# Kernel tuning notes

Hardware: AMD Instinct MI355X
Metric: run time of the kernel (lower is better)

Reference implementation:

```python
import jax, jax.numpy as jnp
import numpy as np

B, T, E, H, L = 2, 2048, 1024, 16, 4
HD = E // H
FF = 4 * E


def setup_inputs() -> dict:
    key = jax.random.key(0)
    ks = jax.random.split(key, 9)
    s = 0.02
    return {
        "x": jax.random.normal(ks[0], (B, T, E), dtype=jnp.float32),
        "Wqkv": jax.random.normal(ks[1], (L, E, 3 * E), dtype=jnp.float32) * s,
        "bqkv": jnp.zeros((L, 3 * E), dtype=jnp.float32),
        "Wproj": jax.random.normal(ks[2], (L, E, E), dtype=jnp.float32) * s,
        "bproj": jnp.zeros((L, E), dtype=jnp.float32),
        "W1": jax.random.normal(ks[3], (L, E, FF), dtype=jnp.float32) * s,
        "b1": jnp.zeros((L, FF), dtype=jnp.float32),
        "W2": jax.random.normal(ks[4], (L, FF, E), dtype=jnp.float32) * s,
        "b2": jnp.zeros((L, E), dtype=jnp.float32),
    }


def _attention(x, Wqkv_l, bqkv_l, Wproj_l, bproj_l):
    # (B,T,E) -> (B,T,E); manual softmax attention as in source
    qkv = x @ Wqkv_l + bqkv_l                      # (B,T,3E)
    q, k, v = jnp.split(qkv, 3, axis=-1)
    q = q.reshape(B, T, H, HD).transpose(0, 2, 1, 3)  # (B,H,T,HD)
    k = k.reshape(B, T, H, HD).transpose(0, 2, 1, 3)
    v = v.reshape(B, T, H, HD).transpose(0, 2, 1, 3)
    att = jnp.einsum("bhqd,bhkd->bhqk", q, k) * (1.0 / np.sqrt(HD))
    att = jax.nn.softmax(att, axis=-1)             # (B,H,T,T)
    y = jnp.einsum("bhqk,bhkd->bhqd", att, v)      # (B,H,T,HD)
    y = y.transpose(0, 2, 1, 3).reshape(B, T, E)
    return y @ Wproj_l + bproj_l


def reference(x, Wqkv, bqkv, Wproj, bproj, W1, b1, W2, b2):
    for l in range(L):
        x = x + _attention(x, Wqkv[l], bqkv[l], Wproj[l], bproj[l])  # residual x+f(x)
        h = jax.nn.gelu(x @ W1[l] + b1[l]) @ W2[l] + b2[l]           # MLP block
        x = x + h
    return x
```

## Files before the change

kernel.cpp:

```cpp
#include <hip/hip_runtime.h>
#include <hip/hip_bf16.h>

#define B_  2
#define T_  2048
#define E_  1024
#define H_  16
#define HD_ 64
#define FF_ 4096
#define L_  4
#define M_  (B_*T_)
#define RS_ (3*E_)

typedef unsigned short u16;
typedef __attribute__((ext_vector_type(8))) short  short8;
typedef __attribute__((ext_vector_type(4))) float  f32x4;

#define QS 0.18033688011112042f

__device__ __forceinline__ u16 f2bf(float f) {
    union { float f; unsigned u; } v; v.f = f;
    unsigned r = (v.u + 0x7fffu + ((v.u >> 16) & 1u)) >> 16;
    return (u16)r;
}
__device__ __forceinline__ u16 f2bf_trunc(float f) {
    union { float f; unsigned u; } v; v.f = f;
    return (u16)(v.u >> 16);
}

__device__ __forceinline__ void gll16(const u16* g, u16* lds) {
    __builtin_amdgcn_global_load_lds(
        (const __attribute__((address_space(1))) unsigned int*)g,
        (__attribute__((address_space(3))) unsigned int*)lds, 16, 0, 0);
}

__global__ __launch_bounds__(256) void transpose_weights(
    const float* __restrict__ Wqkv, const float* __restrict__ Wproj,
    const float* __restrict__ W1,   const float* __restrict__ W2,
    u16* __restrict__ WT) {
    __shared__ float tile[32][33];
    int bid = blockIdx.x;
    const float* src; u16* dst; int K, N, lt;
    if (bid < 3072)      { src = Wqkv;  dst = WT;           K = 1024; N = 3072; lt = bid;        }
    else if (bid < 4096) { src = Wproj; dst = WT + 3145728; K = 1024; N = 1024; lt = bid - 3072; }
    else if (bid < 8192) { src = W1;    dst = WT + 4194304; K = 1024; N = 4096; lt = bid - 4096; }
    else                 { src = W2;    dst = WT + 8388608; K = 4096; N = 1024; lt = bid - 8192; }
    int tpr = N >> 5;
    int ti = lt / tpr, tj = lt % tpr;
    int k0 = ti << 5, n0 = tj << 5;
    int tx = threadIdx.x & 31, ty = threadIdx.x >> 5;
    for (int i = 0; i < 4; i++) {
        int r = ty + (i << 3);
        tile[r][tx] = src[(size_t)(k0 + r) * N + n0 + tx];
    }
    __syncthreads();
    for (int i = 0; i < 4; i++) {
        int r = ty + (i << 3);
        dst[(size_t)(n0 + r) * K + k0 + tx] = f2bf(tile[tx][r]);
    }
}

__global__ __launch_bounds__(256) void convert_kernel(
    const float* __restrict__ in, u16* __restrict__ out, int n4) {
    int i = blockIdx.x * 256 + threadIdx.x;
    if (i < n4) {
        float4 v = ((const float4*)in)[i];
        ushort4 w;
        w.x = f2bf(v.x); w.y = f2bf(v.y); w.z = f2bf(v.z); w.w = f2bf(v.w);
        ((ushort4*)out)[i] = w;
    }
}

template <int EPI>
__global__ __launch_bounds__(512, 4) void gemm_fat(
    const u16* __restrict__ A, const u16* __restrict__ Bt,
    const float* __restrict__ bias, u16* __restrict__ outp,
    int N, int K) {
    __shared__ u16 As[3][128 * 32];
    __shared__ u16 Bs[3][256 * 32];
    int t = threadIdx.x;
    int wid = t >> 6, lane = t & 63;
    int l15 = t & 15, quad = (t >> 4) & 3;
    int wr = wid >> 2, wc = wid & 3;

    int nbx = N >> 8;
    int nwg = nbx << 5;
    int flat = blockIdx.x;
    int q = nwg >> 3;
    int gid = (flat & 7) * q + (flat >> 3);
    int within = gid & 127;
    int m0 = (within >> 2) << 7;
    int n0 = (((gid >> 7) << 2) + (within & 3)) << 8;

    f32x4 acc[4][4];
#pragma unroll
    for (int i = 0; i < 4; i++)
#pragma unroll
        for (int j = 0; j < 4; j++) acc[i][j] = (f32x4){0.f, 0.f, 0.f, 0.f};

    int srow = t >> 2;
    int kch  = (((lane & 3) ^ ((lane >> 3) & 3)) << 3);
    const u16* gA  = &A [(size_t)(m0 + srow) * K + kch];
    const u16* gB0 = &Bt[(size_t)(n0 + srow) * K + kch];
    const u16* gB1 = gB0 + (size_t)128 * K;

    int xo = (l15 >> 1) & 3;
    int abase = (((wr << 6) + l15) << 5) + ((quad ^ xo) << 3);
    int bbase = (((wc << 6) + l15) << 5) + ((quad ^ xo) << 3);

    int nk = K >> 5;

#define STAGE_FAT(buf, ko) do {                                              \
        gll16(gA  + (ko), &As[buf][(wid << 4) << 5]);                        \
        gll16(gB0 + (ko), &Bs[buf][(wid << 4) << 5]);                        \
        gll16(gB1 + (ko), &Bs[buf][((wid << 4) + 128) << 5]);                \
    } while (0)

    STAGE_FAT(0, 0);
    STAGE_FAT(1, 32);

    for (int kk = 0; kk < nk; kk++) {
        if (kk < nk - 1) asm volatile("s_waitcnt vmcnt(3)" ::: "memory");
        else             asm volatile("s_waitcnt vmcnt(0)" ::: "memory");
        __builtin_amdgcn_s_barrier();
        __builtin_amdgcn_sched_barrier(0);

        if (kk + 2 < nk) STAGE_FAT((kk + 2) % 3, (kk + 2) << 5);

        const u16* as = &As[kk % 3][0];
        const u16* bs = &Bs[kk % 3][0];
        short8 af[4], bfr[4];
#pragma unroll
        for (int i = 0; i < 4; i++)
            af[i] = *(const short8*)(as + abase + (i << 9));
#pragma unroll
        for (int j = 0; j < 4; j++)
            bfr[j] = *(const short8*)(bs + bbase + (j << 9));
#pragma unroll
        for (int i = 0; i < 4; i++)
#pragma unroll
            for (int j = 0; j < 4; j++)
                acc[i][j] = __builtin_amdgcn_mfma_f32_16x16x32_bf16(af[i], bfr[j], acc[i][j], 0, 0, 0);
    }
#undef STAGE_FAT

#pragma unroll
    for (int j = 0; j < 4; j++) {
        int gn = n0 + (wc << 6) + (j << 4) + l15;
        float bv = bias[gn];
#pragma unroll
        for (int i = 0; i < 4; i++) {
            int mb = m0 + (wr << 6) + (i << 4) + (quad << 2);
#pragma unroll
            for (int r = 0; r < 4; r++) {
                size_t idx = (size_t)(mb + r) * N + gn;
                float v = acc[i][j][r] + bv;
                if (EPI == 0) {
                    if (gn < E_) v *= QS;
                    outp[idx] = f2bf(v);
                } else {
                    float u  = 0.7978845608028654f * (v + 0.044715f * v * v * v);
                    float th = 1.f - 2.f / (__expf(2.f * u) + 1.f);
                    outp[idx] = f2bf(0.5f * v * (1.f + th));
                }
            }
        }
    }
}

__global__ __launch_bounds__(256) void gemm_n64(
    const u16* __restrict__ A, const u16* __restrict__ Bt,
    const float* __restrict__ bias, const float* __restrict__ res,
    float* __restrict__ outp, u16* __restrict__ out2, int M, int N, int K) {
    __shared__ u16 As[3][128 * 32];
    __shared__ u16 Bs[3][64 * 32];
    int t = threadIdx.x;
    int wid = t >> 6, lane = t & 63;
    int flat = blockIdx.y * gridDim.x + blockIdx.x;
    int gid = ((flat & 7) << 6) + (flat >> 3);
    int within = gid & 127;
    int m0 = (within >> 2) << 7;
    int n0 = (((gid >> 7) << 2) + (within & 3)) << 6;
    int l15 = t & 15, quad = (t >> 4) & 3;
    int wr = wid >> 1, wc = wid & 1;
    f32x4 acc[4][2];
#pragma unroll
    for (int i = 0; i < 4; i++)
#pragma unroll
        for (int j = 0; j < 2; j++) acc[i][j] = (f32x4){0.f, 0.f, 0.f, 0.f};

    int kch = (((lane & 3) ^ ((lane >> 3) & 3)) << 3);
    const u16* gA = &A [(size_t)(m0 + (wid << 5) + (lane >> 2)) * K + kch];
    const u16* gB = &Bt[(size_t)(n0 + (wid << 4) + (lane >> 2)) * K + kch];

    int xo = (l15 >> 1) & 3;
    int abase = (((wr << 6) + l15) << 5) + ((quad ^ xo) << 3);
    int bbase = (((wc << 5) + l15) << 5) + ((quad ^ xo) << 3);

    int nk = K >> 5;

#define STAGE_N64(buf, ko) do {                                              \
        gll16(gA + (ko),                    &As[buf][(wid << 5) << 5]);      \
        gll16(gA + (ko) + (size_t)16 * K,   &As[buf][((wid << 5) + 16) << 5]); \
        gll16(gB + (ko),                    &Bs[buf][(wid << 4) << 5]);      \
    } while (0)

    STAGE_N64(0, 0);
    STAGE_N64(1, 32);

    for (int kk = 0; kk < nk; kk++) {
        if (kk < nk - 1) asm volatile("s_waitcnt vmcnt(3)" ::: "memory");
        else             asm volatile("s_waitcnt vmcnt(0)" ::: "memory");
        __builtin_amdgcn_s_barrier();
        __builtin_amdgcn_sched_barrier(0);

        if (kk + 2 < nk) STAGE_N64((kk + 2) % 3, (kk + 2) << 5);

        const u16* as = &As[kk % 3][0];
        const u16* bs = &Bs[kk % 3][0];
        short8 af[4], bfr[2];
#pragma unroll
        for (int i = 0; i < 4; i++)
            af[i] = *(const short8*)(as + abase + (i << 9));
#pragma unroll
        for (int j = 0; j < 2; j++)
            bfr[j] = *(const short8*)(bs + bbase + (j << 9));
#pragma unroll
        for (int i = 0; i < 4; i++)
#pragma unroll
            for (int j = 0; j < 2; j++)
                acc[i][j] = __builtin_amdgcn_mfma_f32_16x16x32_bf16(
                    af[i], bfr[j], acc[i][j], 0, 0, 0);
    }
#undef STAGE_N64

#pragma unroll
    for (int j = 0; j < 2; j++) {
        int gn = n0 + (wc << 5) + (j << 4) + l15;
        float bv = bias[gn];
#pragma unroll
        for (int i = 0; i < 4; i++) {
            int mb = m0 + (wr << 6) + (i << 4) + (quad << 2);
#pragma unroll
            for (int r = 0; r < 4; r++) {
                size_t idx = (size_t)(mb + r) * N + gn;
                float o = acc[i][j][r] + bv + res[idx];
                outp[idx] = o;
                out2[idx] = f2bf(o);
            }
        }
    }
}

__global__ __launch_bounds__(256) void attn_kernel(
    const u16* __restrict__ qkv, u16* __restrict__ y) {
    __shared__ u16 Ks[2][64 * 64];
    __shared__ u16 Vt[2][64 * 64];
    __shared__ u16 Pb[4][16 * 64];

    int t = threadIdx.x;
    int q0 = blockIdx.x << 6;
    int h  = blockIdx.y;
    int b  = blockIdx.z;
    const u16* bq = qkv + (size_t)b * T_ * RS_;

    int wid = t >> 6, lane = t & 63, l15 = t & 15, quad = (t >> 4) & 3;
    int sw = l15 & 7;
    int ro0 = (l15 << 6) + ((quad ^ sw) << 3);
    int ro1 = ro0 ^ 32;
    int krow = (wid << 4) + (lane >> 3);
    size_t kg0 = (size_t)krow * RS_ + E_ + h * 64 + (((lane & 7) ^ (lane >> 3)) << 3);
    int vkp = t & 31, vdc = t >> 5;
    size_t vg0 = (size_t)(2 * vkp) * RS_ + 2 * E_ + h * 64 + (vdc << 3);
    int vwo[8];
#pragma unroll
    for (int i = 0; i < 8; i++)
        vwo[i] = (((vdc << 3) + i) << 6) + ((((vkp >> 2) ^ i)) << 3) + ((vkp & 3) << 1);
    int pwo[4];
#pragma unroll
    for (int kt = 0; kt < 4; kt++)
        pwo[kt] = (l15 << 6) + ((((kt << 1) | (quad >> 1)) ^ sw) << 3) + ((quad & 1) << 2);
    u16* pw = &Pb[wid][0];

    const u16* qp = bq + (size_t)(q0 + (wid << 4) + l15) * RS_ + h * 64;
    short8 qf0 = *(const short8*)(qp + (quad << 3));
    short8 qf1 = *(const short8*)(qp + (quad << 3) + 32);

    float l = 0.f;
    f32x4 o[4];
#pragma unroll
    for (int dt = 0; dt < 4; dt++) o[dt] = (f32x4){0.f, 0.f, 0.f, 0.f};

    gll16(bq + kg0,            &Ks[0][(wid << 4) << 6]);
    gll16(bq + kg0 + 8 * RS_,  &Ks[0][((wid << 4) + 8) << 6]);
    {
        union { uint4 q; u16 u[8]; } a_, b_;
        a_.q = *(const uint4*)(bq + vg0);
        b_.q = *(const uint4*)(bq + vg0 + RS_);
#pragma unroll
        for (int i = 0; i < 8; i++) {
            unsigned pk = (unsigned)a_.u[i] | ((unsigned)b_.u[i] << 16);
            *(unsigned*)(&Vt[0][0] + vwo[i]) = pk;
        }
    }

#define ATTN_CHUNK(KSB, VTB, KSN, VTN, C0) do {                                \
    __syncthreads();                           \
    int cn_ = (C0) + 64;                                                       \
    uint4 v0_, v1_;                                                            \
    bool pf_ = (cn_ < T_);                                                     \
    if (pf_) {                                                                 \
        size_t cb_ = (size_t)cn_ * RS_;                                        \
        gll16(bq + cb_ + kg0,           (KSN) + ((wid << 4) << 6));            \
        gll16(bq + cb_ + kg0 + 8 * RS_, (KSN) + (((wid << 4) + 8) << 6));      \
        v0_ = *(const uint4*)(bq + cb_ + vg0);                                 \
        v1_ = *(const uint4*)(bq + cb_ + vg0 + RS_);                           \
    }                                                                          \
    f32x4 s_[4];                                                               \
    _Pragma("unroll")                                                          \
    for (int kt = 0; kt < 4; kt++) {                                           \
        short8 ka0 = *(const short8*)((KSB) + (kt << 10) + ro0);               \
        short8 ka1 = *(const short8*)((KSB) + (kt << 10) + ro1);               \
        f32x4 z = (f32x4){0.f, 0.f, 0.f, 0.f};                                 \
        z = __builtin_amdgcn_mfma_f32_16x16x32_bf16(ka0, qf0, z, 0, 0, 0);     \
        z = __builtin_amdgcn_mfma_f32_16x16x32_bf16(ka1, qf1, z, 0, 0, 0);     \
        s_[kt] = z;                                                            \
    }                                                                          \
    float rsum_ = 0.f;                                                         \
    _Pragma("unroll")                                                          \
    for (int kt = 0; kt < 4; kt++) {                                           \
        float p0_ = __builtin_amdgcn_exp2f(s_[kt][0]);                         \
        float p1_ = __builtin_amdgcn_exp2f(s_[kt][1]);                         \
        float p2_ = __builtin_amdgcn_exp2f(s_[kt][2]);                         \
        float p3_ = __builtin_amdgcn_exp2f(s_[kt][3]);                         \
        rsum_ += (p0_ + p1_) + (p2_ + p3_);                                    \
        ushort4 w_;                                                            \
        w_.x = f2bf_trunc(p0_); w_.y = f2bf_trunc(p1_);                        \
        w_.z = f2bf_trunc(p2_); w_.w = f2bf_trunc(p3_);                        \
        *(ushort4*)(pw + pwo[kt]) = w_;                                        \
    }                                                                          \
    rsum_ += __shfl_xor(rsum_, 16);                                            \
    rsum_ += __shfl_xor(rsum_, 32);                                            \
    l += rsum_;                                                                \
    __threadfence_block();                   \
    short8 pb0 = *(const short8*)(pw + ro0);                                   \
    short8 pb1 = *(const short8*)(pw + ro1);                                   \
    _Pragma("unroll")                                                          \
    for (int dt = 0; dt < 4; dt++) {                                           \
        short8 vf0 = *(const short8*)((VTB) + (dt << 10) + ro0);               \
        short8 vf1 = *(const short8*)((VTB) + (dt << 10) + ro1);               \
        o[dt] = __builtin_amdgcn_mfma_f32_16x16x32_bf16(vf0, pb0, o[dt], 0, 0, 0); \
        o[dt] = __builtin_amdgcn_mfma_f32_16x16x32_bf16(vf1, pb1, o[dt], 0, 0, 0); \
    }                                                                          \
    if (pf_) {                                                                 \
        union { uint4 q; u16 u[8]; } a_, b_;                                   \
        a_.q = v0_; b_.q = v1_;                                                \
        _Pragma("unroll")                                                      \
        for (int i = 0; i < 8; i++) {                                          \
            unsigned pk_ = (unsigned)a_.u[i] | ((unsigned)b_.u[i] << 16);      \
            *(unsigned*)((VTN) + vwo[i]) = pk_;                                \
        }                                                                      \
    }                                                                          \
} while (0)

    for (int c0 = 0; c0 < T_; c0 += 128) {
        ATTN_CHUNK(&Ks[0][0], &Vt[0][0], &Ks[1][0], &Vt[1][0], c0);
        ATTN_CHUNK(&Ks[1][0], &Vt[1][0], &Ks[0][0], &Vt[0][0], c0 + 64);
    }
#undef ATTN_CHUNK

    float rl = __builtin_amdgcn_rcpf(l);
    size_t yrow = ((size_t)b * T_ + q0 + (wid << 4) + l15) * E_ + h * 64;
#pragma unroll
    for (int dt = 0; dt < 4; dt++) {
        ushort4 w;
        w.x = f2bf(o[dt][0] * rl); w.y = f2bf(o[dt][1] * rl);
        w.z = f2bf(o[dt][2] * rl); w.w = f2bf(o[dt][3] * rl);
        *(ushort4*)&y[yrow + (dt << 4) + (quad << 2)] = w;
    }
}

extern "C" void kernel_launch(void* const* d_in, const int* in_sizes, int n_in,
                              void* d_out, int out_size, void* d_ws, size_t ws_size,
                              hipStream_t stream) {
    const float* x_in  = (const float*)d_in[0];
    const float* Wqkv  = (const float*)d_in[1];
    const float* bqkv  = (const float*)d_in[2];
    const float* Wproj = (const float*)d_in[3];
    const float* bproj = (const float*)d_in[4];
    const float* W1    = (const float*)d_in[5];
    const float* b1    = (const float*)d_in[6];
    const float* W2    = (const float*)d_in[7];
    const float* b2    = (const float*)d_in[8];
    float* out = (float*)d_out;

    u16* WT   = (u16*)d_ws;
    u16* qkvb = WT   + 12582912;
    u16* yb   = qkvb + 12582912;
    u16* hb   = yb   + 4194304;
    u16* xb   = hb   + 16777216;

    convert_kernel<<<4096, 256, 0, stream>>>(x_in, xb, M_ * E_ / 4);

    for (int l = 0; l < L_; l++) {
        transpose_weights<<<12288, 256, 0, stream>>>(
            Wqkv + (size_t)l * E_ * 3 * E_, Wproj + (size_t)l * E_ * E_,
            W1 + (size_t)l * E_ * FF_, W2 + (size_t)l * FF_ * E_, WT);

        const float* xcur = (l == 0) ? x_in : out;

        gemm_fat<0><<<dim3(384), 512, 0, stream>>>(
            xb, WT, bqkv + l * 3 * E_, qkvb, 3 * E_, E_);

        attn_kernel<<<dim3(T_ / 64, H_, B_), 256, 0, stream>>>(qkvb, yb);

        gemm_n64<<<dim3(16, 32), 256, 0, stream>>>(
            yb, WT + 3145728, bproj + l * E_, xcur, out, xb, M_, E_, E_);

        gemm_fat<2><<<dim3(512), 512, 0, stream>>>(
            xb, WT + 4194304, b1 + l * FF_, hb, FF_, E_);

        gemm_n64<<<dim3(16, 32), 256, 0, stream>>>(
            hb, WT + 8388608, b2 + l * E_, out, out, xb, M_, E_, FF_);
    }
}
```

Before: 1.184 ms.

## Split-K the N=1024 GEMMs across two warp groups and retile the QKV GEMM

The projection and MLP-down GEMMs (N=1024) become gemm_n64_sk: 512 threads, where two groups of four waves each cover half of K for the same 128x64 tile and then reduce through LDS before the residual epilogue. The aim is more waves in flight per block on the long-K FF2 GEMM, which otherwise leaves the 512-tile grid with low occupancy. The QKV GEMM moves from gemm_fat to a new 128x128 tile kernel (gemm_sq) with 768 blocks of 256 threads and launch bounds of 3 blocks per CU, trading tile size for better CU fill. The costs are extra LDS traffic and barriers for the split-K reduction and smaller tiles with less reuse for QKV.

```diff
diff --git a/kernel.cpp b/kernel.cpp
--- a/kernel.cpp
+++ b/kernel.cpp
@@ -167,45 +167,145 @@
     }
 }
 
-__global__ __launch_bounds__(256) void gemm_n64(
+template <int EPI>
+__global__ __launch_bounds__(256, 3) void gemm_sq(
+    const u16* __restrict__ A, const u16* __restrict__ Bt,
+    const float* __restrict__ bias, u16* __restrict__ outp,
+    int N, int K) {
+    __shared__ u16 As[3][128 * 32];
+    __shared__ u16 Bs[3][128 * 32];
+    int t = threadIdx.x;
+    int wid = t >> 6, lane = t & 63;
+    int l15 = t & 15, quad = (t >> 4) & 3;
+    int wr = wid >> 1, wc = wid & 1;
+
+    int nbx = N >> 7;
+    int nwg = nbx << 5;
+    int flat = blockIdx.x;
+    int q = nwg >> 3;
+    int gid = (flat & 7) * q + (flat >> 3);
+    int within = gid & 127;
+    int m0 = (within >> 2) << 7;
+    int n0 = (((gid >> 7) << 2) + (within & 3)) << 7;
+
+    f32x4 acc[4][4];
+#pragma unroll
+    for (int i = 0; i < 4; i++)
+#pragma unroll
+        for (int j = 0; j < 4; j++) acc[i][j] = (f32x4){0.f, 0.f, 0.f, 0.f};
+
+    int kch = (((lane & 3) ^ ((lane >> 3) & 3)) << 3);
+    const u16* gA = &A [(size_t)(m0 + (wid << 5) + (lane >> 2)) * K + kch];
+    const u16* gB = &Bt[(size_t)(n0 + (wid << 5) + (lane >> 2)) * K + kch];
+
+    int xo = (l15 >> 1) & 3;
+    int abase = (((wr << 6) + l15) << 5) + ((quad ^ xo) << 3);
+    int bbase = (((wc << 6) + l15) << 5) + ((quad ^ xo) << 3);
+
+    int nk = K >> 5;
+
+#define STAGE_SQ(buf, ko) do {                                                \
+        gll16(gA + (ko),                  &As[buf][((wid << 5)     ) << 5]);  \
+        gll16(gA + (ko) + (size_t)16 * K, &As[buf][((wid << 5) + 16) << 5]);  \
+        gll16(gB + (ko),                  &Bs[buf][((wid << 5)     ) << 5]);  \
+        gll16(gB + (ko) + (size_t)16 * K, &Bs[buf][((wid << 5) + 16) << 5]);  \
+    } while (0)
+
+    STAGE_SQ(0, 0);
+    STAGE_SQ(1, 32);
+
+    for (int kk = 0; kk < nk; kk++) {
+        if (kk < nk - 1) asm volatile("s_waitcnt vmcnt(4)" ::: "memory");
+        else             asm volatile("s_waitcnt vmcnt(0)" ::: "memory");
+        __builtin_amdgcn_s_barrier();
+        __builtin_amdgcn_sched_barrier(0);
+
+        if (kk + 2 < nk) STAGE_SQ((kk + 2) % 3, (kk + 2) << 5);
+
+        const u16* as = &As[kk % 3][0];
+        const u16* bs = &Bs[kk % 3][0];
+        short8 af[4], bfr[4];
+#pragma unroll
+        for (int i = 0; i < 4; i++)
+            af[i] = *(const short8*)(as + abase + (i << 9));
+#pragma unroll
+        for (int j = 0; j < 4; j++)
+            bfr[j] = *(const short8*)(bs + bbase + (j << 9));
+#pragma unroll
+        for (int i = 0; i < 4; i++)
+#pragma unroll
+            for (int j = 0; j < 4; j++)
+                acc[i][j] = __builtin_amdgcn_mfma_f32_16x16x32_bf16(af[i], bfr[j], acc[i][j], 0, 0, 0);
+    }
+#undef STAGE_SQ
+
+#pragma unroll
+    for (int j = 0; j < 4; j++) {
+        int gn = n0 + (wc << 6) + (j << 4) + l15;
+        float bv = bias[gn];
+#pragma unroll
+        for (int i = 0; i < 4; i++) {
+            int mb = m0 + (wr << 6) + (i << 4) + (quad << 2);
+#pragma unroll
+            for (int r = 0; r < 4; r++) {
+                size_t idx = (size_t)(mb + r) * N + gn;
+                float v = acc[i][j][r] + bv;
+                if (EPI == 0) {
+                    if (gn < E_) v *= QS;
+                    outp[idx] = f2bf(v);
+                } else {
+                    float u  = 0.7978845608028654f * (v + 0.044715f * v * v * v);
+                    float th = 1.f - 2.f / (__expf(2.f * u) + 1.f);
+                    outp[idx] = f2bf(0.5f * v * (1.f + th));
+                }
+            }
+        }
+    }
+}
+
+__global__ __launch_bounds__(512, 4) void gemm_n64_sk(
     const u16* __restrict__ A, const u16* __restrict__ Bt,
     const float* __restrict__ bias, const float* __restrict__ res,
-    float* __restrict__ outp, u16* __restrict__ out2, int M, int N, int K) {
-    __shared__ u16 As[3][128 * 32];
-    __shared__ u16 Bs[3][64 * 32];
+    float* __restrict__ outp, u16* __restrict__ out2, int N, int K) {
+    __shared__ u16 As[2][3][128 * 32];
+    __shared__ u16 Bs[2][3][64 * 32];
     int t = threadIdx.x;
     int wid = t >> 6, lane = t & 63;
-    int flat = blockIdx.y * gridDim.x + blockIdx.x;
+    int grp = wid >> 2, w4 = wid & 3;
+    int l15 = t & 15, quad = (t >> 4) & 3;
+    int wr = w4 >> 1, wc = w4 & 1;
+
+    int flat = blockIdx.x;
     int gid = ((flat & 7) << 6) + (flat >> 3);
     int within = gid & 127;
     int m0 = (within >> 2) << 7;
     int n0 = (((gid >> 7) << 2) + (within & 3)) << 6;
-    int l15 = t & 15, quad = (t >> 4) & 3;
-    int wr = wid >> 1, wc = wid & 1;
+
     f32x4 acc[4][2];
 #pragma unroll
     for (int i = 0; i < 4; i++)
 #pragma unroll
         for (int j = 0; j < 2; j++) acc[i][j] = (f32x4){0.f, 0.f, 0.f, 0.f};
 
+    int kh = K >> 1;
     int kch = (((lane & 3) ^ ((lane >> 3) & 3)) << 3);
-    const u16* gA = &A [(size_t)(m0 + (wid << 5) + (lane >> 2)) * K + kch];
-    const u16* gB = &Bt[(size_t)(n0 + (wid << 4) + (lane >> 2)) * K + kch];
+    const u16* gA = &A [(size_t)(m0 + (w4 << 5) + (lane >> 2)) * K + (size_t)grp * kh + kch];
+    const u16* gB = &Bt[(size_t)(n0 + (w4 << 4) + (lane >> 2)) * K + (size_t)grp * kh + kch];
 
     int xo = (l15 >> 1) & 3;
     int abase = (((wr << 6) + l15) << 5) + ((quad ^ xo) << 3);
     int bbase = (((wc << 5) + l15) << 5) + ((quad ^ xo) << 3);
 
-    int nk = K >> 5;
-
-#define STAGE_N64(buf, ko) do {                                              \
-        gll16(gA + (ko),                    &As[buf][(wid << 5) << 5]);      \
-        gll16(gA + (ko) + (size_t)16 * K,   &As[buf][((wid << 5) + 16) << 5]); \
-        gll16(gB + (ko),                    &Bs[buf][(wid << 4) << 5]);      \
+    int nk = kh >> 5;
+
+#define STAGE_SK(buf, ko) do {                                                 \
+        gll16(gA + (ko),                  &As[grp][buf][((w4 << 5)     ) << 5]); \
+        gll16(gA + (ko) + (size_t)16 * K, &As[grp][buf][((w4 << 5) + 16) << 5]); \
+        gll16(gB + (ko),                  &Bs[grp][buf][((w4 << 4)     ) << 5]); \
     } while (0)
 
-    STAGE_N64(0, 0);
-    STAGE_N64(1, 32);
+    STAGE_SK(0, 0);
+    STAGE_SK(1, 32);
 
     for (int kk = 0; kk < nk; kk++) {
         if (kk < nk - 1) asm volatile("s_waitcnt vmcnt(3)" ::: "memory");
@@ -213,10 +313,10 @@
         __builtin_amdgcn_s_barrier();
         __builtin_amdgcn_sched_barrier(0);
 
-        if (kk + 2 < nk) STAGE_N64((kk + 2) % 3, (kk + 2) << 5);
-
-        const u16* as = &As[kk % 3][0];
-        const u16* bs = &Bs[kk % 3][0];
+        if (kk + 2 < nk) STAGE_SK((kk + 2) % 3, (kk + 2) << 5);
+
+        const u16* as = &As[grp][kk % 3][0];
+        const u16* bs = &Bs[grp][kk % 3][0];
         short8 af[4], bfr[2];
 #pragma unroll
         for (int i = 0; i < 4; i++)
@@ -231,23 +331,43 @@
                 acc[i][j] = __builtin_amdgcn_mfma_f32_16x16x32_bf16(
                     af[i], bfr[j], acc[i][j], 0, 0, 0);
     }
-#undef STAGE_N64
-
-#pragma unroll
-    for (int j = 0; j < 2; j++) {
-        int gn = n0 + (wc << 5) + (j << 4) + l15;
-        float bv = bias[gn];
-#pragma unroll
-        for (int i = 0; i < 4; i++) {
-            int mb = m0 + (wr << 6) + (i << 4) + (quad << 2);
-#pragma unroll
-            for (int r = 0; r < 4; r++) {
-                size_t idx = (size_t)(mb + r) * N + gn;
-                float o = acc[i][j][r] + bv + res[idx];
-                outp[idx] = o;
-                out2[idx] = f2bf(o);
+#undef STAGE_SK
+
+    float* part = (float*)&As[1][0][0];
+    int ti = t & 255;
+    __syncthreads();
+#pragma unroll
+    for (int half = 0; half < 2; half++) {
+        if (grp == 1) {
+#pragma unroll
+            for (int i2 = 0; i2 < 2; i2++)
+#pragma unroll
+                for (int j = 0; j < 2; j++)
+                    *(f32x4*)&part[(ti << 4) + (i2 << 3) + (j << 2)] =
+                        acc[(half << 1) + i2][j];
+        }
+        __syncthreads();
+        if (grp == 0) {
+#pragma unroll
+            for (int i2 = 0; i2 < 2; i2++) {
+                int i = (half << 1) + i2;
+#pragma unroll
+                for (int j = 0; j < 2; j++) {
+                    f32x4 p = *(const f32x4*)&part[(ti << 4) + (i2 << 3) + (j << 2)];
+                    int gn = n0 + (wc << 5) + (j << 4) + l15;
+                    float bv = bias[gn];
+                    int mb = m0 + (wr << 6) + (i << 4) + (quad << 2);
+#pragma unroll
+                    for (int r = 0; r < 4; r++) {
+                        size_t idx = (size_t)(mb + r) * N + gn;
+                        float o = acc[i][j][r] + p[r] + bv + res[idx];
+                        outp[idx] = o;
+                        out2[idx] = f2bf(o);
+                    }
+                }
             }
         }
+        __syncthreads();
     }
 }
 
@@ -408,18 +528,18 @@
 
         const float* xcur = (l == 0) ? x_in : out;
 
-        gemm_fat<0><<<dim3(384), 512, 0, stream>>>(
+        gemm_sq<0><<<dim3(768), 256, 0, stream>>>(
             xb, WT, bqkv + l * 3 * E_, qkvb, 3 * E_, E_);
 
         attn_kernel<<<dim3(T_ / 64, H_, B_), 256, 0, stream>>>(qkvb, yb);
 
-        gemm_n64<<<dim3(16, 32), 256, 0, stream>>>(
-            yb, WT + 3145728, bproj + l * E_, xcur, out, xb, M_, E_, E_);
+        gemm_n64_sk<<<dim3(512), 512, 0, stream>>>(
+            yb, WT + 3145728, bproj + l * E_, xcur, out, xb, E_, E_);
 
         gemm_fat<2><<<dim3(512), 512, 0, stream>>>(
             xb, WT + 4194304, b1 + l * FF_, hb, FF_, E_);
 
-        gemm_n64<<<dim3(16, 32), 256, 0, stream>>>(
-            hb, WT + 8388608, b2 + l * E_, out, out, xb, M_, E_, FF_);
-    }
-}
+        gemm_n64_sk<<<dim3(512), 512, 0, stream>>>(
+            hb, WT + 8388608, b2 + l * E_, out, out, xb, E_, FF_);
+    }
+}
```

After: 1.138 ms. 1.04x faster.
